# Kernel optimization log

Hardware: AMD Instinct MI355X
Metric: run time of the kernel (lower is better)

## Reference

```python
import jax, jax.numpy as jnp
import numpy as np

B, S, H, N, D = 2, 2048, 1024, 16, 64  # batch, seq, hidden, heads, head_size
PAD = -30000.0


def setup_inputs() -> dict:
    key = jax.random.key(0)
    kx, kqkv, kout, krpe = jax.random.split(key, 4)
    x = jax.random.normal(kx, (B, S, H), jnp.float32)
    qkv = jax.random.normal(kqkv, (H, 3, N, D), jnp.float32) * H ** (-0.5)
    out_w = jax.random.normal(kout, (N, D, H), jnp.float32) * (N * D) ** (-0.5)
    # rpe_bias is zero-init in torch; use small randn so the bias path is exercised
    rpe_bias = jax.random.normal(krpe, (N, S), jnp.float32) * 0.02
    return {"x": x, "qkv": qkv, "out_w": out_w, "rpe_bias": rpe_bias}


def reference(x, qkv, out_w, rpe_bias):
    # q, k, v: [B, N, S, D]
    q, k, v = jnp.einsum('bsx,xMnd->Mbnsd', x, qkv)
    s = x.shape[1]
    a = jnp.einsum('bnsd,bntd->bnst', q, k) * q.shape[-1] ** (-0.5)
    # cumulative relative-position bias: bias[n, i, j] = cumsum(rpe)[n, i-j] for i>=j,
    # PAD otherwise (exactly what to_tril produces on the row-broadcast cumsum).
    cum = jnp.cumsum(rpe_bias[:, :s], axis=-1)            # [N, S]
    rel = jnp.arange(s)[:, None] - jnp.arange(s)[None, :]  # [S, S], i - j
    bias = jnp.where(rel >= 0, cum[:, jnp.clip(rel, 0)], PAD)  # [N, S, S]
    a = jax.nn.softmax(a + bias, axis=-1)
    mix = jnp.einsum('bnst,bntd->bnsd', a, v)
    return jnp.einsum('bnsd,ndx->bsx', mix, out_w)
```

## Files before the change

kernel.cpp:

```cpp
#include <hip/hip_runtime.h>
#include <hip/hip_bf16.h>
#include <cstdint>
#include <cstddef>

#define B_   2
#define S_   2048
#define H_   1024
#define NH   16
#define DH   64
#define LOG2E 1.4426950408889634f
#define SCALE2 (0.125f * LOG2E)

typedef __hip_bfloat16 bf16;
typedef short bf16x8 __attribute__((ext_vector_type(8)));
typedef float f32x4 __attribute__((ext_vector_type(4)));

#define MFMA16(a, b, c) __builtin_amdgcn_mfma_f32_16x16x32_bf16((a), (b), (c), 0, 0, 0)

__device__ __forceinline__ void async16(const void* g, void* l) {
  __builtin_amdgcn_global_load_lds(
      (const __attribute__((address_space(1))) void*)g,
      (__attribute__((address_space(3))) void*)l,
      16, 0, 0);
}

__device__ __forceinline__ void tr_body(const float* __restrict__ src,
                                        bf16* __restrict__ dst, int R, int C,
                                        int c0, int r0, bf16 (*tile)[33], int tid) {
  int tx = tid & 31, ty = tid >> 5;
  for (int i = 0; i < 32; i += 8)
    tile[ty + i][tx] = __float2bfloat16(src[(size_t)(r0 + ty + i) * C + c0 + tx]);
  __syncthreads();
  for (int i = 0; i < 32; i += 8)
    dst[(size_t)(c0 + ty + i) * R + r0 + tx] = tile[tx][ty + i];
}

__global__ __launch_bounds__(256)
void prep(const float* __restrict__ x, bf16* __restrict__ xb,
          const float* __restrict__ qkv, bf16* __restrict__ qkvT,
          const float* __restrict__ outw, bf16* __restrict__ outwT,
          const float* __restrict__ rpe, float* __restrict__ cum) {
  __shared__ char pm[2176] __attribute__((aligned(16)));
  const int L = blockIdx.x, tid = threadIdx.x;
  if (L < 4096) {
    int i = (L * 256 + tid) * 4;
    float4 v = *(const float4*)(x + i);
    bf16 o[4] = {__float2bfloat16(v.x), __float2bfloat16(v.y),
                 __float2bfloat16(v.z), __float2bfloat16(v.w)};
    *(uint64_t*)(xb + i) = *(const uint64_t*)o;
  } else if (L < 7168) {
    int t = L - 4096;
    int cx = t % 96, ry = t / 96;
    tr_body(qkv, qkvT, 1024, 3072, cx * 32, ry * 32, (bf16(*)[33])pm, tid);
  } else if (L < 8192) {
    int t = L - 7168;
    int cx = t & 31, ry = t >> 5;
    tr_body(outw, outwT, 1024, 1024, cx * 32, ry * 32, (bf16(*)[33])pm, tid);
  } else {
    float* ssum = (float*)pm;
    int n = L - 8192;
    float loc[8];
    float s = 0.f;
    int base = tid * 8;
#pragma unroll
    for (int u = 0; u < 8; ++u) {
      loc[u] = rpe[n * S_ + base + u];
      s += loc[u];
    }
    ssum[tid] = s;
    __syncthreads();
    float own = s;
    for (int off = 1; off < 256; off <<= 1) {
      float v = (tid >= off) ? ssum[tid - off] : 0.f;
      __syncthreads();
      ssum[tid] += v;
      __syncthreads();
    }
    float run = ssum[tid] - own;
#pragma unroll
    for (int u = 0; u < 8; ++u) {
      run += loc[u];
      cum[n * S_ + base + u] = run * LOG2E;
    }
  }
}

template <int MODE>
__global__ __launch_bounds__(256, MODE == 0 ? 3 : 2)
void gemm_bt(const bf16* __restrict__ A, const bf16* __restrict__ Bt,
             bf16* __restrict__ C0, bf16* __restrict__ C1, bf16* __restrict__ C2,
             float* __restrict__ F0) {
  __shared__ char smem[MODE == 0 ? 36864 : 16384] __attribute__((aligned(16)));
  bf16* As = (bf16*)smem;
  bf16* Bs = (bf16*)(smem + 8192);
  const int tid = threadIdx.x, lane = tid & 63, w = tid >> 6;
  const int lr = lane & 15, lq = lane >> 4;
  const int m0 = blockIdx.y * 128, n0 = blockIdx.x * 128;
  const int wm = (w & 1) * 64, wn = (w >> 1) * 64;

  f32x4 acc[4][4] = {};

  for (int k0 = 0; k0 < 1024; k0 += 32) {
    __syncthreads();
    for (int t = 0; t < 2; ++t) {
      int c = (t * 4 + w) * 64 + lane;
      int row = c >> 2, ch = c & 3;
      int k8 = (ch ^ ((row >> 1) & 3)) * 8;
      async16(A + (size_t)(m0 + row) * 1024 + k0 + k8,
              (char*)As + (size_t)(t * 4 + w) * 1024 + lane * 16);
      async16(Bt + (size_t)(n0 + row) * 1024 + k0 + k8,
              (char*)Bs + (size_t)(t * 4 + w) * 1024 + lane * 16);
    }
    __syncthreads();
    bf16x8 af[4], bfr[4];
#pragma unroll
    for (int mt = 0; mt < 4; ++mt) {
      int row = wm + mt * 16 + lr;
      af[mt] = *(const bf16x8*)(As + row * 32 + ((lq ^ ((row >> 1) & 3)) << 3));
    }
#pragma unroll
    for (int nt = 0; nt < 4; ++nt) {
      int row = wn + nt * 16 + lr;
      bfr[nt] = *(const bf16x8*)(Bs + row * 32 + ((lq ^ ((row >> 1) & 3)) << 3));
    }
#pragma unroll
    for (int mt = 0; mt < 4; ++mt)
#pragma unroll
      for (int nt = 0; nt < 4; ++nt)
        acc[mt][nt] = MFMA16(af[mt], bfr[nt], acc[mt][nt]);
  }

  if (MODE == 0) {
    __syncthreads();
    bf16* E = (bf16*)smem + w * (64 * 72);
    const int cbase = n0 + wn;
    const int mm = cbase >> 10, nn = (cbase >> 6) & 15;
    const int bb = (m0 + wm) >> 11;
    const int sbase = (m0 + wm) & 2047;
    if (mm < 2) {
#pragma unroll
      for (int mt = 0; mt < 4; ++mt)
#pragma unroll
        for (int nt = 0; nt < 4; ++nt)
#pragma unroll
          for (int r = 0; r < 4; ++r)
            E[(mt * 16 + lq * 4 + r) * 72 + nt * 16 + lr] =
                __float2bfloat16(acc[mt][nt][r]);
      bf16* dst = (mm == 0 ? C0 : C1) +
                  ((size_t)(bb * NH + nn) * S_ + sbase) * DH;
#pragma unroll
      for (int it = 0; it < 8; ++it) {
        int c = it * 64 + lane;
        int rw = c >> 3, c8 = c & 7;
        *(uint4*)(dst + (size_t)rw * DH + c8 * 8) =
            *(const uint4*)(E + rw * 72 + c8 * 8);
      }
    } else {
#pragma unroll
      for (int mt = 0; mt < 4; ++mt)
#pragma unroll
        for (int nt = 0; nt < 4; ++nt)
#pragma unroll
          for (int r = 0; r < 4; ++r)
            E[(nt * 16 + lr) * 72 + mt * 16 + lq * 4 + r] =
                __float2bfloat16(acc[mt][nt][r]);
      bf16* dst = C2 + (size_t)(bb * NH + nn) * DH * S_;
#pragma unroll
      for (int it = 0; it < 8; ++it) {
        int c = it * 64 + lane;
        int dr = c >> 3, c8 = c & 7;
        *(uint4*)(dst + (size_t)dr * S_ + sbase + c8 * 8) =
            *(const uint4*)(E + dr * 72 + c8 * 8);
      }
    }
  } else {
#pragma unroll
    for (int mt = 0; mt < 4; ++mt)
#pragma unroll
      for (int nt = 0; nt < 4; ++nt)
#pragma unroll
        for (int r = 0; r < 4; ++r) {
          int rM = m0 + wm + mt * 16 + lq * 4 + r;
          int cN = n0 + wn + nt * 16 + lr;
          F0[(size_t)rM * 1024 + cN] = acc[mt][nt][r];
        }
  }
}

__global__ __launch_bounds__(256, 3)
void fa_kernel(const bf16* __restrict__ q, const bf16* __restrict__ k,
               const bf16* __restrict__ vt, const float* __restrict__ cum,
               bf16* __restrict__ mix) {
  __shared__ char smem[51200] __attribute__((aligned(16)));
  bf16* Ps = (bf16*)(smem + 32768);
  float* cumbuf = (float*)(smem + 50176);

  const int tid = threadIdx.x, lane = tid & 63, w = tid >> 6;
  const int lr = lane & 15, lq = lane >> 4;

  const int L = blockIdx.x;
  const int xcd = L & 7, slot = L >> 3;
  const int bn = xcd + 8 * (slot >> 5);
  const int ti = 31 - (slot & 31);
  const int n = bn & (NH - 1);
  const int b = bn >> 4;
  const float* cumn = cum + n * S_;

  const int i0 = ti * 64;
  const int nj = (ti >> 1) + 1;

  const bf16* qbase = q + ((size_t)bn * S_ + i0 + w * 16) * DH;
  bf16x8 qf[2];
#pragma unroll
  for (int kt = 0; kt < 2; ++kt)
    qf[kt] = *(const bf16x8*)(qbase + lr * DH + kt * 32 + lq * 8);

  bf16x8 ones;
#pragma unroll
  for (int u = 0; u < 8; ++u) ones[u] = (short)0x3F80;

  f32x4 oacc[4] = {};
  f32x4 lacc = {};
  const int iloc = w * 16 + lr;

  for (int jt = 0; jt < nj; ++jt) {
    const int j0 = jt * 128;
    const bool diag = (jt == nj - 1);
    __syncthreads();

    const char* ksrc = (const char*)(k + ((size_t)bn * S_ + j0) * DH);
#pragma unroll
    for (int t = 0; t < 4; ++t) {
      int cb = t * 4 + w;
      int row = cb * 8 + (lane >> 3);
      int cs = (lane & 7) ^ (row & 7);
      async16(ksrc + row * 128 + cs * 16, smem + cb * 1024 + lane * 16);
    }
    const char* vsrc = (const char*)(vt + (size_t)bn * DH * S_);
#pragma unroll
    for (int t = 0; t < 4; ++t) {
      int cb = t * 4 + w;
      int row = cb * 4 + (lane >> 4);
      int cs = (lane & 15) ^ (row & 15);
      async16(vsrc + (size_t)row * (S_ * 2) + j0 * 2 + cs * 16,
              smem + 16384 + cb * 1024 + lane * 16);
    }
    {
      int src = i0 - j0 - 127 + tid;
      src = src < 0 ? 0 : (src > S_ - 1 ? S_ - 1 : src);
      cumbuf[tid] = cumn[src];
    }
    __syncthreads();

    f32x4 sa[8] = {};
#pragma unroll
    for (int kt = 0; kt < 2; ++kt)
#pragma unroll
      for (int nt = 0; nt < 8; ++nt) {
        int krow = nt * 16 + lr;
        bf16x8 kf = *(const bf16x8*)(smem + krow * 128 +
                        (((kt * 4 + lq) ^ (krow & 7)) << 4));
        sa[nt] = MFMA16(kf, qf[kt], sa[nt]);
      }

    const int doff = i0 - j0;
    if (!diag) {
#pragma unroll
      for (int nt = 0; nt < 8; ++nt) {
        bf16 pk[4];
#pragma unroll
        for (int r = 0; r < 4; ++r) {
          int rel = iloc - nt * 16 - lq * 4 - r;
          float p = exp2f(sa[nt][r] * SCALE2 + cumbuf[127 + rel]);
          pk[r] = __float2bfloat16(p);
        }
        *(uint64_t*)(Ps + iloc * 136 + nt * 16 + lq * 4) = *(const uint64_t*)pk;
      }
    } else {
#pragma unroll
      for (int nt = 0; nt < 8; ++nt) {
        bf16 pk[4];
#pragma unroll
        for (int r = 0; r < 4; ++r) {
          int rel = iloc - nt * 16 - lq * 4 - r;
          float p = (doff + rel >= 0)
                        ? exp2f(sa[nt][r] * SCALE2 + cumbuf[127 + rel])
                        : 0.f;
          pk[r] = __float2bfloat16(p);
        }
        *(uint64_t*)(Ps + iloc * 136 + nt * 16 + lq * 4) = *(const uint64_t*)pk;
      }
    }

#pragma unroll
    for (int kt2 = 0; kt2 < 4; ++kt2) {
      bf16x8 pf = *(const bf16x8*)(Ps + (w * 16 + lr) * 136 + kt2 * 32 + lq * 8);
      lacc = MFMA16(pf, ones, lacc);
#pragma unroll
      for (int dt = 0; dt < 4; ++dt) {
        int vrow = dt * 16 + lr;
        bf16x8 vf = *(const bf16x8*)(smem + 16384 + vrow * 256 +
                        (((kt2 * 4 + lq) ^ (vrow & 15)) << 4));
        oacc[dt] = MFMA16(pf, vf, oacc[dt]);
      }
    }
  }

#pragma unroll
  for (int dt = 0; dt < 4; ++dt)
#pragma unroll
    for (int r = 0; r < 4; ++r) {
      int i = i0 + w * 16 + lq * 4 + r;
      int d = dt * 16 + lr;
      mix[((size_t)(b * S_ + i) * NH + n) * DH + d] =
          __float2bfloat16(oacc[dt][r] / lacc[r]);
    }
}

extern "C" void kernel_launch(void* const* d_in, const int* in_sizes, int n_in,
                              void* d_out, int out_size, void* d_ws, size_t ws_size,
                              hipStream_t stream) {
  const float* x     = (const float*)d_in[0];
  const float* qkv   = (const float*)d_in[1];
  const float* out_w = (const float*)d_in[2];
  const float* rpe   = (const float*)d_in[3];
  float* out = (float*)d_out;

  char* ws = (char*)d_ws;
  bf16* qkvT  = (bf16*)(ws + 0);
  bf16* outwT = (bf16*)(ws + 6291456);
  bf16* xb    = (bf16*)(ws + 8388608);
  bf16* qb    = (bf16*)(ws + 16777216);
  bf16* kb    = (bf16*)(ws + 25165824);
  bf16* vtb   = (bf16*)(ws + 33554432);
  bf16* mixb  = (bf16*)(ws + 41943040);
  float* cum  = (float*)(ws + 50331648);

  prep<<<8208, 256, 0, stream>>>(x, xb, qkv, qkvT, out_w, outwT, rpe, cum);
  gemm_bt<0><<<dim3(3072 / 128, 4096 / 128), 256, 0, stream>>>(xb, qkvT, qb, kb, vtb, nullptr);
  fa_kernel<<<1024, 256, 0, stream>>>(qb, kb, vtb, cum, mixb);
  gemm_bt<1><<<dim3(1024 / 128, 4096 / 128), 256, 0, stream>>>(mixb, outwT, nullptr, nullptr, nullptr, out);
}
```

Measured before the change: 196.6 us.

## Switch attention kernel to 32x32x16 MFMA with 2x2 warp tiling

Rewrites the flash-attention inner loop to use 32x32x16 bf16 MFMAs instead of 16x16x32. Warps are arranged as a 2x2 grid over query rows and key columns for QK^T and over query rows and head dims for PV, so P now goes through a swizzled shared buffer with an extra barrier. The cumsum bias buffer is stored as four shifted copies so each lane can read a 4-wide vector instead of doing scalar loads. The goal is fewer MFMA issues and less LDS traffic per tile, at the cost of an additional __syncthreads per iteration and more shared memory.

Result: slower. 214.1 us (+8.9%).

```diff
diff --git a/kernel.cpp b/kernel.cpp
--- a/kernel.cpp
+++ b/kernel.cpp
@@ -14,8 +14,10 @@
 typedef __hip_bfloat16 bf16;
 typedef short bf16x8 __attribute__((ext_vector_type(8)));
 typedef float f32x4 __attribute__((ext_vector_type(4)));
+typedef float f32x16 __attribute__((ext_vector_type(16)));
 
 #define MFMA16(a, b, c) __builtin_amdgcn_mfma_f32_16x16x32_bf16((a), (b), (c), 0, 0, 0)
+#define MFMA32(a, b, c) __builtin_amdgcn_mfma_f32_32x32x16_bf16((a), (b), (c), 0, 0, 0)
 
 __device__ __forceinline__ void async16(const void* g, void* l) {
   __builtin_amdgcn_global_load_lds(
@@ -191,12 +193,11 @@
 void fa_kernel(const bf16* __restrict__ q, const bf16* __restrict__ k,
                const bf16* __restrict__ vt, const float* __restrict__ cum,
                bf16* __restrict__ mix) {
-  __shared__ char smem[51200] __attribute__((aligned(16)));
-  bf16* Ps = (bf16*)(smem + 32768);
-  float* cumbuf = (float*)(smem + 50176);
+  __shared__ char smem[52224] __attribute__((aligned(16)));
+  float* cumS = (float*)(smem + 49152);
 
   const int tid = threadIdx.x, lane = tid & 63, w = tid >> 6;
-  const int lr = lane & 15, lq = lane >> 4;
+  const int l31 = lane & 31, lh = lane >> 5;
 
   const int L = blockIdx.x;
   const int xcd = L & 7, slot = L >> 3;
@@ -209,23 +210,28 @@
   const int i0 = ti * 64;
   const int nj = (ti >> 1) + 1;
 
-  const bf16* qbase = q + ((size_t)bn * S_ + i0 + w * 16) * DH;
-  bf16x8 qf[2];
-#pragma unroll
-  for (int kt = 0; kt < 2; ++kt)
-    qf[kt] = *(const bf16x8*)(qbase + lr * DH + kt * 32 + lq * 8);
+  const int ib = (w & 1) * 32;
+  const int db = (w >> 1) * 32;
+  const int jbw = (w >> 1) * 64;
+  const int iloc = ib + l31;
+
+  const bf16* qrow = q + ((size_t)bn * S_ + i0 + iloc) * DH;
+  bf16x8 qf[4];
+#pragma unroll
+  for (int dc = 0; dc < 4; ++dc)
+    qf[dc] = *(const bf16x8*)(qrow + dc * 16 + lh * 8);
 
   bf16x8 ones;
 #pragma unroll
   for (int u = 0; u < 8; ++u) ones[u] = (short)0x3F80;
 
-  f32x4 oacc[4] = {};
-  f32x4 lacc = {};
-  const int iloc = w * 16 + lr;
+  f32x16 oacc = {};
+  f32x16 lacc = {};
 
   for (int jt = 0; jt < nj; ++jt) {
     const int j0 = jt * 128;
     const bool diag = (jt == nj - 1);
+    const int doff = i0 - j0;
     __syncthreads();
 
     const char* ksrc = (const char*)(k + ((size_t)bn * S_ + j0) * DH);
@@ -245,76 +251,91 @@
       async16(vsrc + (size_t)row * (S_ * 2) + j0 * 2 + cs * 16,
               smem + 16384 + cb * 1024 + lane * 16);
     }
-    {
-      int src = i0 - j0 - 127 + tid;
-      src = src < 0 ? 0 : (src > S_ - 1 ? S_ - 1 : src);
-      cumbuf[tid] = cumn[src];
-    }
-    __syncthreads();
-
-    f32x4 sa[8] = {};
-#pragma unroll
-    for (int kt = 0; kt < 2; ++kt)
-#pragma unroll
-      for (int nt = 0; nt < 8; ++nt) {
-        int krow = nt * 16 + lr;
-        bf16x8 kf = *(const bf16x8*)(smem + krow * 128 +
-                        (((kt * 4 + lq) ^ (krow & 7)) << 4));
-        sa[nt] = MFMA16(kf, qf[kt], sa[nt]);
+    if (tid < 192) {
+      int base = i0 - j0 - 127 + tid;
+#pragma unroll
+      for (int p = 0; p < 4; ++p) {
+        int src = base + p;
+        src = src < 0 ? 0 : (src > S_ - 1 ? S_ - 1 : src);
+        cumS[p * 192 + tid] = cumn[src];
       }
-
-    const int doff = i0 - j0;
+    }
+    __syncthreads();
+
+    f32x16 sa2[2] = {};
+#pragma unroll
+    for (int dc = 0; dc < 4; ++dc)
+#pragma unroll
+      for (int t32 = 0; t32 < 2; ++t32) {
+        int row = jbw + t32 * 32 + l31;
+        bf16x8 kf = *(const bf16x8*)(smem + row * 128 +
+                        (((dc * 2 + lh) ^ (row & 7)) << 4));
+        sa2[t32] = MFMA32(kf, qf[dc], sa2[t32]);
+      }
+
     if (!diag) {
 #pragma unroll
-      for (int nt = 0; nt < 8; ++nt) {
-        bf16 pk[4];
-#pragma unroll
-        for (int r = 0; r < 4; ++r) {
-          int rel = iloc - nt * 16 - lq * 4 - r;
-          float p = exp2f(sa[nt][r] * SCALE2 + cumbuf[127 + rel]);
-          pk[r] = __float2bfloat16(p);
+      for (int t32 = 0; t32 < 2; ++t32)
+#pragma unroll
+        for (int qq = 0; qq < 4; ++qq) {
+          int jl = jbw + t32 * 32 + qq * 8 + lh * 4;
+          int Xm3 = 124 + iloc - jl;
+          int p = Xm3 & 3, b0 = Xm3 & ~3;
+          f32x4 cv = *(const f32x4*)(cumS + p * 192 + b0);
+          bf16 pk[4];
+#pragma unroll
+          for (int m = 0; m < 4; ++m)
+            pk[m] = __float2bfloat16(
+                exp2f(sa2[t32][qq * 4 + m] * SCALE2 + cv[3 - m]));
+          int c = (jbw >> 3) + t32 * 4 + qq;
+          *(uint64_t*)(smem + 32768 + iloc * 256 +
+                       ((c ^ (iloc & 15)) << 4) + lh * 8) = *(const uint64_t*)pk;
         }
-        *(uint64_t*)(Ps + iloc * 136 + nt * 16 + lq * 4) = *(const uint64_t*)pk;
-      }
     } else {
 #pragma unroll
-      for (int nt = 0; nt < 8; ++nt) {
-        bf16 pk[4];
-#pragma unroll
-        for (int r = 0; r < 4; ++r) {
-          int rel = iloc - nt * 16 - lq * 4 - r;
-          float p = (doff + rel >= 0)
-                        ? exp2f(sa[nt][r] * SCALE2 + cumbuf[127 + rel])
-                        : 0.f;
-          pk[r] = __float2bfloat16(p);
+      for (int t32 = 0; t32 < 2; ++t32)
+#pragma unroll
+        for (int qq = 0; qq < 4; ++qq) {
+          int jl = jbw + t32 * 32 + qq * 8 + lh * 4;
+          int Xm3 = 124 + iloc - jl;
+          int p = Xm3 & 3, b0 = Xm3 & ~3;
+          f32x4 cv = *(const f32x4*)(cumS + p * 192 + b0);
+          bf16 pk[4];
+#pragma unroll
+          for (int m = 0; m < 4; ++m) {
+            float pv = (doff + iloc - jl - m >= 0)
+                           ? exp2f(sa2[t32][qq * 4 + m] * SCALE2 + cv[3 - m])
+                           : 0.f;
+            pk[m] = __float2bfloat16(pv);
+          }
+          int c = (jbw >> 3) + t32 * 4 + qq;
+          *(uint64_t*)(smem + 32768 + iloc * 256 +
+                       ((c ^ (iloc & 15)) << 4) + lh * 8) = *(const uint64_t*)pk;
         }
-        *(uint64_t*)(Ps + iloc * 136 + nt * 16 + lq * 4) = *(const uint64_t*)pk;
-      }
-    }
-
-#pragma unroll
-    for (int kt2 = 0; kt2 < 4; ++kt2) {
-      bf16x8 pf = *(const bf16x8*)(Ps + (w * 16 + lr) * 136 + kt2 * 32 + lq * 8);
-      lacc = MFMA16(pf, ones, lacc);
-#pragma unroll
-      for (int dt = 0; dt < 4; ++dt) {
-        int vrow = dt * 16 + lr;
-        bf16x8 vf = *(const bf16x8*)(smem + 16384 + vrow * 256 +
-                        (((kt2 * 4 + lq) ^ (vrow & 15)) << 4));
-        oacc[dt] = MFMA16(pf, vf, oacc[dt]);
-      }
-    }
-  }
-
-#pragma unroll
-  for (int dt = 0; dt < 4; ++dt)
-#pragma unroll
-    for (int r = 0; r < 4; ++r) {
-      int i = i0 + w * 16 + lq * 4 + r;
-      int d = dt * 16 + lr;
-      mix[((size_t)(b * S_ + i) * NH + n) * DH + d] =
-          __float2bfloat16(oacc[dt][r] / lacc[r]);
-    }
+    }
+
+    __syncthreads();
+
+#pragma unroll
+    for (int kc = 0; kc < 8; ++kc) {
+      int rr = ib + l31;
+      bf16x8 pf = *(const bf16x8*)(smem + 32768 + rr * 256 +
+                      (((kc * 2 + lh) ^ (rr & 15)) << 4));
+      lacc = MFMA32(pf, ones, lacc);
+      int dd = db + l31;
+      bf16x8 vf = *(const bf16x8*)(smem + 16384 + dd * 256 +
+                      (((kc * 2 + lh) ^ (dd & 15)) << 4));
+      oacc = MFMA32(pf, vf, oacc);
+    }
+  }
+
+#pragma unroll
+  for (int r = 0; r < 16; ++r) {
+    int i = i0 + ib + (r & 3) + 8 * (r >> 2) + 4 * lh;
+    int d = db + l31;
+    mix[((size_t)(b * S_ + i) * NH + n) * DH + d] =
+        __float2bfloat16(oacc[r] / lacc[r]);
+  }
 }
 
 extern "C" void kernel_launch(void* const* d_in, const int* in_sizes, int n_in,
```

## Read K fragments directly from global in attention and narrow output GEMM tile

Applied to the files above, without the earlier changes.

The attention kernel no longer stages K tiles in LDS. Each wave loads its K fragments straight from global memory (relying on L1/L2 reuse), which shrinks shared memory to about 34 KB and raises the occupancy target from 3 to 4 blocks. Separately, the output projection GEMM now uses 128x64 tiles instead of 128x128, doubling its grid to 512 blocks for better CU coverage. The cost is uncoalesced, redundant global reads of K in the attention inner loop and less operand reuse per block in the output GEMM.

New measurement: 267.3 us. +36.0%, slower.

```diff
diff --git a/kernel.cpp b/kernel.cpp
--- a/kernel.cpp
+++ b/kernel.cpp
@@ -90,43 +90,52 @@
 void gemm_bt(const bf16* __restrict__ A, const bf16* __restrict__ Bt,
              bf16* __restrict__ C0, bf16* __restrict__ C1, bf16* __restrict__ C2,
              float* __restrict__ F0) {
-  __shared__ char smem[MODE == 0 ? 36864 : 16384] __attribute__((aligned(16)));
+  constexpr int NT = (MODE == 0) ? 4 : 2;
+  constexpr int NB = NT * 32;
+  __shared__ char smem[MODE == 0 ? 36864 : 12288] __attribute__((aligned(16)));
   bf16* As = (bf16*)smem;
   bf16* Bs = (bf16*)(smem + 8192);
   const int tid = threadIdx.x, lane = tid & 63, w = tid >> 6;
   const int lr = lane & 15, lq = lane >> 4;
-  const int m0 = blockIdx.y * 128, n0 = blockIdx.x * 128;
-  const int wm = (w & 1) * 64, wn = (w >> 1) * 64;
-
-  f32x4 acc[4][4] = {};
+  const int m0 = blockIdx.y * 128, n0 = blockIdx.x * NB;
+  const int wm = (w & 1) * 64, wn = (w >> 1) * (NT * 16);
+
+  f32x4 acc[4][NT] = {};
 
   for (int k0 = 0; k0 < 1024; k0 += 32) {
     __syncthreads();
+#pragma unroll
     for (int t = 0; t < 2; ++t) {
       int c = (t * 4 + w) * 64 + lane;
       int row = c >> 2, ch = c & 3;
       int k8 = (ch ^ ((row >> 1) & 3)) * 8;
       async16(A + (size_t)(m0 + row) * 1024 + k0 + k8,
               (char*)As + (size_t)(t * 4 + w) * 1024 + lane * 16);
+    }
+#pragma unroll
+    for (int t = 0; t < NB / 64; ++t) {
+      int c = (t * 4 + w) * 64 + lane;
+      int row = c >> 2, ch = c & 3;
+      int k8 = (ch ^ ((row >> 1) & 3)) * 8;
       async16(Bt + (size_t)(n0 + row) * 1024 + k0 + k8,
               (char*)Bs + (size_t)(t * 4 + w) * 1024 + lane * 16);
     }
     __syncthreads();
-    bf16x8 af[4], bfr[4];
+    bf16x8 af[4], bfr[NT];
 #pragma unroll
     for (int mt = 0; mt < 4; ++mt) {
       int row = wm + mt * 16 + lr;
       af[mt] = *(const bf16x8*)(As + row * 32 + ((lq ^ ((row >> 1) & 3)) << 3));
     }
 #pragma unroll
-    for (int nt = 0; nt < 4; ++nt) {
+    for (int nt = 0; nt < NT; ++nt) {
       int row = wn + nt * 16 + lr;
       bfr[nt] = *(const bf16x8*)(Bs + row * 32 + ((lq ^ ((row >> 1) & 3)) << 3));
     }
 #pragma unroll
     for (int mt = 0; mt < 4; ++mt)
 #pragma unroll
-      for (int nt = 0; nt < 4; ++nt)
+      for (int nt = 0; nt < NT; ++nt)
         acc[mt][nt] = MFMA16(af[mt], bfr[nt], acc[mt][nt]);
   }
 
@@ -177,7 +186,7 @@
 #pragma unroll
     for (int mt = 0; mt < 4; ++mt)
 #pragma unroll
-      for (int nt = 0; nt < 4; ++nt)
+      for (int nt = 0; nt < NT; ++nt)
 #pragma unroll
         for (int r = 0; r < 4; ++r) {
           int rM = m0 + wm + mt * 16 + lq * 4 + r;
@@ -187,13 +196,13 @@
   }
 }
 
-__global__ __launch_bounds__(256, 3)
+__global__ __launch_bounds__(256, 4)
 void fa_kernel(const bf16* __restrict__ q, const bf16* __restrict__ k,
                const bf16* __restrict__ vt, const float* __restrict__ cum,
                bf16* __restrict__ mix) {
-  __shared__ char smem[51200] __attribute__((aligned(16)));
-  bf16* Ps = (bf16*)(smem + 32768);
-  float* cumbuf = (float*)(smem + 50176);
+  __shared__ char smem[34816] __attribute__((aligned(16)));
+  bf16* Ps = (bf16*)(smem + 16384);
+  float* cumbuf = (float*)(smem + 33792);
 
   const int tid = threadIdx.x, lane = tid & 63, w = tid >> 6;
   const int lr = lane & 15, lq = lane >> 4;
@@ -222,20 +231,13 @@
   f32x4 oacc[4] = {};
   f32x4 lacc = {};
   const int iloc = w * 16 + lr;
+  const bf16* kbase = k + (size_t)bn * S_ * DH;
 
   for (int jt = 0; jt < nj; ++jt) {
     const int j0 = jt * 128;
     const bool diag = (jt == nj - 1);
     __syncthreads();
 
-    const char* ksrc = (const char*)(k + ((size_t)bn * S_ + j0) * DH);
-#pragma unroll
-    for (int t = 0; t < 4; ++t) {
-      int cb = t * 4 + w;
-      int row = cb * 8 + (lane >> 3);
-      int cs = (lane & 7) ^ (row & 7);
-      async16(ksrc + row * 128 + cs * 16, smem + cb * 1024 + lane * 16);
-    }
     const char* vsrc = (const char*)(vt + (size_t)bn * DH * S_);
 #pragma unroll
     for (int t = 0; t < 4; ++t) {
@@ -243,7 +245,7 @@
       int row = cb * 4 + (lane >> 4);
       int cs = (lane & 15) ^ (row & 15);
       async16(vsrc + (size_t)row * (S_ * 2) + j0 * 2 + cs * 16,
-              smem + 16384 + cb * 1024 + lane * 16);
+              smem + cb * 1024 + lane * 16);
     }
     {
       int src = i0 - j0 - 127 + tid;
@@ -252,14 +254,13 @@
     }
     __syncthreads();
 
+    const bf16* ksrc = kbase + (size_t)j0 * DH;
     f32x4 sa[8] = {};
 #pragma unroll
     for (int kt = 0; kt < 2; ++kt)
 #pragma unroll
       for (int nt = 0; nt < 8; ++nt) {
-        int krow = nt * 16 + lr;
-        bf16x8 kf = *(const bf16x8*)(smem + krow * 128 +
-                        (((kt * 4 + lq) ^ (krow & 7)) << 4));
+        bf16x8 kf = *(const bf16x8*)(ksrc + (nt * 16 + lr) * DH + kt * 32 + lq * 8);
         sa[nt] = MFMA16(kf, qf[kt], sa[nt]);
       }
 
@@ -299,7 +300,7 @@
 #pragma unroll
       for (int dt = 0; dt < 4; ++dt) {
         int vrow = dt * 16 + lr;
-        bf16x8 vf = *(const bf16x8*)(smem + 16384 + vrow * 256 +
+        bf16x8 vf = *(const bf16x8*)(smem + vrow * 256 +
                         (((kt2 * 4 + lq) ^ (vrow & 15)) << 4));
         oacc[dt] = MFMA16(pf, vf, oacc[dt]);
       }
@@ -339,5 +340,5 @@
   prep<<<8208, 256, 0, stream>>>(x, xb, qkv, qkvT, out_w, outwT, rpe, cum);
   gemm_bt<0><<<dim3(3072 / 128, 4096 / 128), 256, 0, stream>>>(xb, qkvT, qb, kb, vtb, nullptr);
   fa_kernel<<<1024, 256, 0, stream>>>(qb, kb, vtb, cum, mixb);
-  gemm_bt<1><<<dim3(1024 / 128, 4096 / 128), 256, 0, stream>>>(mixb, outwT, nullptr, nullptr, nullptr, out);
-}
+  gemm_bt<1><<<dim3(1024 / 64, 4096 / 128), 256, 0, stream>>>(mixb, outwT, nullptr, nullptr, nullptr, out);
+}
```
